# Kernel tuning notes

Hardware: AMD Instinct MI355X
Metric: run time of the kernel (lower is better)

The kernel has to match this reference:

```python
import jax, jax.numpy as jnp
import numpy as np

MARGIN = 0.3  # init kwarg, mode='norm'


def _pairwise_dist(X):
    # squared euclidean distances, then safe sqrt (matches euc_dist(X.t()).sqrt())
    sq = jnp.sum(X * X, axis=1)                      # [n]
    d2 = sq[:, None] + sq[None, :] - 2.0 * (X @ X.T)  # [n, n]
    d2 = jnp.maximum(d2, 0.0)
    # safe sqrt: avoid inf derivative at 0 (diagonal); forward value identical
    return jnp.where(d2 > 0.0, jnp.sqrt(jnp.where(d2 > 0.0, d2, 1.0)), 0.0)


def setup_inputs() -> dict:
    key = jax.random.key(0)
    kx, ky = jax.random.split(key)
    X = jax.random.normal(kx, (4096, 2048), dtype=jnp.float32)
    Y = jax.random.randint(ky, (4096,), 0, 128, dtype=jnp.int64)
    return {"X": X, "Y": Y}


def reference(X, Y):
    dist = _pairwise_dist(X)                         # [n, n]
    mask = Y[:, None] == Y[None, :]                  # same-identity mask [n, n]
    inf = jnp.array(jnp.inf, dtype=dist.dtype)
    # hardest positive per anchor: max over same-label entries
    dist_ap = jnp.max(jnp.where(mask, dist, -inf), axis=1)  # [n]
    # hardest negative per anchor: min over different-label entries
    dist_an = jnp.min(jnp.where(mask, inf, dist), axis=1)   # [n]
    # mode == 'norm': mean hinge
    return jnp.mean(jnp.maximum(dist_ap - dist_an + MARGIN, 0.0))
```

## Files before the change

### kernel.cpp

```cpp
#include <hip/hip_runtime.h>
#include <hip/hip_bf16.h>
#include <hip/hip_fp8.h>

typedef __attribute__((ext_vector_type(4))) int i32x4;
typedef __attribute__((ext_vector_type(8))) int i32x8;
typedef __attribute__((ext_vector_type(16))) float f32x16;

#define MARGIN 0.3f
#define BIGF 3.0e38f

__device__ __forceinline__ void gl2lds16(const void* g, void* l) {
    __builtin_amdgcn_global_load_lds(
        (const __attribute__((address_space(1))) void*)g,
        (__attribute__((address_space(3))) void*)l,
        16, 0, 0);
}

__global__ __launch_bounds__(256) void convert_norm_kernel(
    const float* __restrict__ X, unsigned char* __restrict__ Xq,
    float* __restrict__ nrm, unsigned* __restrict__ ap,
    unsigned* __restrict__ an, unsigned* __restrict__ cnt, int K) {
    const int wave = threadIdx.x >> 6, lane = threadIdx.x & 63;
    const int row = blockIdx.x * 4 + wave;
    const float* xr = X + (size_t)row * K;
    unsigned char* xqr = Xq + (size_t)row * K;
    float s = 0.0f;
    for (int c = lane * 8; c < K; c += 64 * 8) {
        float4 v0 = *(const float4*)(xr + c);
        float4 v1 = *(const float4*)(xr + c + 4);
        float f[8] = {v0.x, v0.y, v0.z, v0.w, v1.x, v1.y, v1.z, v1.w};
        union { unsigned char b[8]; uint2 u; } p;
#pragma unroll
        for (int i = 0; i < 8; i++) {
            __hip_fp8_e4m3 q(f[i]);
            p.b[i] = q.__x;
            float d = (float)q;
            s += d * d;
        }
        *(uint2*)(xqr + c) = p.u;
    }
    for (int off = 32; off > 0; off >>= 1) s += __shfl_xor(s, off, 64);
    if (lane == 0) {
        nrm[row] = s;
        ap[row] = 0u;
        an[row] = 0x7F800000u;
        if (row == 0) *cnt = 0u;
    }
}

__global__ __launch_bounds__(256, 4) void gemm_reduce_kernel(
    const unsigned char* __restrict__ Xq, const float* __restrict__ nrm,
    const int* __restrict__ Y, unsigned* __restrict__ ap,
    unsigned* __restrict__ an, unsigned* __restrict__ cnt,
    float* __restrict__ out, int N, int K) {
    __shared__ __align__(16) unsigned char sA[128 * 128];
    __shared__ __align__(16) unsigned char sB[128 * 128];
    __shared__ int sYr[128], sYc[128];
    __shared__ float sNr[128], sNc[128];
    __shared__ float redmax[4][64], redmin[4][64];
    __shared__ float lsum[4];
    __shared__ unsigned s_done;

    const int tid = threadIdx.x;
    const int wave = tid >> 6;
    const int lane = tid & 63;
    const int m = lane & 31;
    const int h = lane >> 5;
    const int wr = wave >> 1;
    const int wc = wave & 1;

    const int NB = N >> 7;
    const int rowBase = (blockIdx.x >> 5) * 128;
    const int colBase = (blockIdx.x & (NB - 1)) * 128;

    if (tid < 128) {
        sYr[tid] = Y[rowBase + tid];
        sNr[tid] = nrm[rowBase + tid];
    } else {
        int t = tid - 128;
        sYc[t] = Y[colBase + t];
        sNc[t] = nrm[colBase + t];
    }

    f32x16 acc[2][2];
#pragma unroll
    for (int si = 0; si < 2; si++)
#pragma unroll
        for (int sj = 0; sj < 2; sj++)
#pragma unroll
            for (int rr = 0; rr < 16; rr++) acc[si][sj][rr] = 0.0f;

    const int rsub = lane >> 3;
    const int jc = (lane & 7) ^ rsub;
    const unsigned char* gA = Xq + (size_t)(rowBase + wave * 32 + rsub) * K;
    const unsigned char* gB = Xq + (size_t)(colBase + wave * 32 + rsub) * K;
    unsigned char* lA = sA + wave * 4096;
    unsigned char* lB = sB + wave * 4096;
    const size_t g8 = (size_t)8 * K;

    const int e2 = (m & 7) ^ ((m >> 3) & 3);
    const int nit = K >> 7;

    for (int it = 0; it < nit; it++) {
        const size_t go = (size_t)it * 128;
#pragma unroll
        for (int g = 0; g < 4; g++) {
            gl2lds16(gA + go + g * g8 + ((jc ^ g) << 4), lA + g * 1024);
            gl2lds16(gB + go + g * g8 + ((jc ^ g) << 4), lB + g * 1024);
        }
        __syncthreads();

#pragma unroll
        for (int s = 0; s < 2; s++) {
            const int c0 = s * 4 + h * 2;
            i32x8 af[2], bf[2];
#pragma unroll
            for (int si = 0; si < 2; si++) {
                const unsigned char* base = sA + (wr * 64 + si * 32 + m) * 128;
                i32x4 lo = *(const i32x4*)(base + (((c0) ^ e2) << 4));
                i32x4 hi = *(const i32x4*)(base + (((c0 + 1) ^ e2) << 4));
                af[si] = __builtin_shufflevector(lo, hi, 0, 1, 2, 3, 4, 5, 6, 7);
            }
#pragma unroll
            for (int sj = 0; sj < 2; sj++) {
                const unsigned char* base = sB + (wc * 64 + sj * 32 + m) * 128;
                i32x4 lo = *(const i32x4*)(base + (((c0) ^ e2) << 4));
                i32x4 hi = *(const i32x4*)(base + (((c0 + 1) ^ e2) << 4));
                bf[sj] = __builtin_shufflevector(lo, hi, 0, 1, 2, 3, 4, 5, 6, 7);
            }
#pragma unroll
            for (int si = 0; si < 2; si++)
#pragma unroll
                for (int sj = 0; sj < 2; sj++)
                    acc[si][sj] = __builtin_amdgcn_mfma_scale_f32_32x32x64_f8f6f4(
                        af[si], bf[sj], acc[si][sj], 0 ,
                        0 , 0, 127 ,
                        0, 127 );
        }
        __syncthreads();
    }

#pragma unroll
    for (int si = 0; si < 2; si++)
#pragma unroll
        for (int reg = 0; reg < 16; reg++) {
            const int row64 = si * 32 + (reg & 3) + 8 * (reg >> 2) + 4 * h;
            const int rIdx = wr * 64 + row64;
            const int yr = sYr[rIdx];
            const float nr = sNr[rIdx];
            float dp = -1.0f, dn = BIGF;
#pragma unroll
            for (int sj = 0; sj < 2; sj++) {
                const int cIdx = wc * 64 + sj * 32 + m;
                float d2 = nr + sNc[cIdx] - 2.0f * acc[si][sj][reg];
                float d = sqrtf(fmaxf(d2, 0.0f));
                bool same = (yr == sYc[cIdx]);
                dp = fmaxf(dp, same ? d : -1.0f);
                dn = fminf(dn, same ? BIGF : d);
            }
            for (int off = 1; off < 32; off <<= 1) {
                dp = fmaxf(dp, __shfl_xor(dp, off, 64));
                dn = fminf(dn, __shfl_xor(dn, off, 64));
            }
            if (m == 0) {
                redmax[wave][row64] = dp;
                redmin[wave][row64] = dn;
            }
        }
    __syncthreads();

    if (tid < 128) {
        const int wr2 = tid >> 6, r64 = tid & 63;
        float mx = fmaxf(redmax[wr2 * 2][r64], redmax[wr2 * 2 + 1][r64]);
        float mn = fminf(redmin[wr2 * 2][r64], redmin[wr2 * 2 + 1][r64]);
        atomicMax(&ap[rowBase + tid], __float_as_uint(fmaxf(mx, 0.0f)));
        atomicMin(&an[rowBase + tid], __float_as_uint(mn));
    }

    __syncthreads();
    if (tid == 0) {
        __threadfence();
        s_done = atomicAdd(cnt, 1u);
    }
    __syncthreads();
    if (s_done == gridDim.x - 1) {
        __threadfence();
        float s = 0.0f;
        for (int i = tid; i < N; i += 256) {
            unsigned ua = __hip_atomic_load(&ap[i], __ATOMIC_RELAXED,
                                            __HIP_MEMORY_SCOPE_AGENT);
            unsigned ub = __hip_atomic_load(&an[i], __ATOMIC_RELAXED,
                                            __HIP_MEMORY_SCOPE_AGENT);
            s += fmaxf(__uint_as_float(ua) - __uint_as_float(ub) + MARGIN, 0.0f);
        }
        for (int off = 32; off > 0; off >>= 1) s += __shfl_xor(s, off, 64);
        if (lane == 0) lsum[wave] = s;
        __syncthreads();
        if (tid == 0)
            out[0] = (lsum[0] + lsum[1] + lsum[2] + lsum[3]) / (float)N;
    }
}

extern "C" void kernel_launch(void* const* d_in, const int* in_sizes, int n_in,
                              void* d_out, int out_size, void* d_ws, size_t ws_size,
                              hipStream_t stream) {
    const float* X = (const float*)d_in[0];
    const int* Y = (const int*)d_in[1];
    float* out = (float*)d_out;
    const int N = in_sizes[1];
    const int K = in_sizes[0] / N;

    char* ws = (char*)d_ws;
    unsigned char* Xq = (unsigned char*)ws;
    float* nrm = (float*)(ws + (size_t)N * K);
    unsigned* ap = (unsigned*)((char*)nrm + (size_t)N * 4);
    unsigned* an = (unsigned*)((char*)ap + (size_t)N * 4);
    unsigned* cnt = (unsigned*)((char*)an + (size_t)N * 4);

    convert_norm_kernel<<<N / 4, 256, 0, stream>>>(X, Xq, nrm, ap, an, cnt, K);
    const int NB = N / 128;
    gemm_reduce_kernel<<<NB * NB, 256, 0, stream>>>(Xq, nrm, Y, ap, an, cnt,
                                                    out, N, K);
}
```

Before: 132.9 us.

## Pre-swizzle FP8 operands into MFMA fragment layout and load directly from global

The conversion kernel now writes the FP8 matrix in a fragment-packed layout: 32-row panels, with each 64-wide K slice stored contiguously per lane. The GEMM drops LDS staging and per-iteration barriers, and each lane loads its 32-byte MFMA operands straight from global memory. This removes LDS traffic and synchronisation but gives up in-block reuse, so every wave fetches its own A and B fragments and relies on L2/L1 for reuse. An explicit barrier was added after the label and norm shared-memory loads.

```diff
diff --git a/kernel.cpp b/kernel.cpp
--- a/kernel.cpp
+++ b/kernel.cpp
@@ -9,21 +9,27 @@
 #define MARGIN 0.3f
 #define BIGF 3.0e38f
 
-__device__ __forceinline__ void gl2lds16(const void* g, void* l) {
-    __builtin_amdgcn_global_load_lds(
-        (const __attribute__((address_space(1))) void*)g,
-        (__attribute__((address_space(3))) void*)l,
-        16, 0, 0);
+__device__ __forceinline__ f32x16 mx_mfma(i32x8 a, i32x8 b, f32x16 c) {
+    return __builtin_amdgcn_mfma_scale_f32_32x32x64_f8f6f4(
+        a, b, c, 0 , 0 ,
+        0, 127 , 0, 127 );
+}
+
+__device__ __forceinline__ i32x8 ld32(const unsigned char* p) {
+    i32x4 lo = *(const i32x4*)p;
+    i32x4 hi = *(const i32x4*)(p + 16);
+    return __builtin_shufflevector(lo, hi, 0, 1, 2, 3, 4, 5, 6, 7);
 }
 
 __global__ __launch_bounds__(256) void convert_norm_kernel(
-    const float* __restrict__ X, unsigned char* __restrict__ Xq,
+    const float* __restrict__ X, unsigned char* __restrict__ Xf,
     float* __restrict__ nrm, unsigned* __restrict__ ap,
     unsigned* __restrict__ an, unsigned* __restrict__ cnt, int K) {
     const int wave = threadIdx.x >> 6, lane = threadIdx.x & 63;
     const int row = blockIdx.x * 4 + wave;
     const float* xr = X + (size_t)row * K;
-    unsigned char* xqr = Xq + (size_t)row * K;
+    const size_t pbase = ((size_t)(row >> 5)) << 16;
+    const int rsub = row & 31;
     float s = 0.0f;
     for (int c = lane * 8; c < K; c += 64 * 8) {
         float4 v0 = *(const float4*)(xr + c);
@@ -37,7 +43,10 @@
             float d = (float)q;
             s += d * d;
         }
-        *(uint2*)(xqr + c) = p.u;
+        const int lslot = rsub + (((c >> 5) & 1) << 5);
+        unsigned char* dst = Xf + pbase + ((size_t)(c >> 6) << 11)
+                             + (lslot << 5) + (c & 31);
+        *(uint2*)dst = p.u;
     }
     for (int off = 32; off > 0; off >>= 1) s += __shfl_xor(s, off, 64);
     if (lane == 0) {
@@ -49,12 +58,10 @@
 }
 
 __global__ __launch_bounds__(256, 4) void gemm_reduce_kernel(
-    const unsigned char* __restrict__ Xq, const float* __restrict__ nrm,
+    const unsigned char* __restrict__ Xf, const float* __restrict__ nrm,
     const int* __restrict__ Y, unsigned* __restrict__ ap,
     unsigned* __restrict__ an, unsigned* __restrict__ cnt,
     float* __restrict__ out, int N, int K) {
-    __shared__ __align__(16) unsigned char sA[128 * 128];
-    __shared__ __align__(16) unsigned char sB[128 * 128];
     __shared__ int sYr[128], sYc[128];
     __shared__ float sNr[128], sNc[128];
     __shared__ float redmax[4][64], redmin[4][64];
@@ -81,6 +88,7 @@
         sYc[t] = Y[colBase + t];
         sNc[t] = nrm[colBase + t];
     }
+    __syncthreads();
 
     f32x16 acc[2][2];
 #pragma unroll
@@ -90,54 +98,25 @@
 #pragma unroll
             for (int rr = 0; rr < 16; rr++) acc[si][sj][rr] = 0.0f;
 
-    const int rsub = lane >> 3;
-    const int jc = (lane & 7) ^ rsub;
-    const unsigned char* gA = Xq + (size_t)(rowBase + wave * 32 + rsub) * K;
-    const unsigned char* gB = Xq + (size_t)(colBase + wave * 32 + rsub) * K;
-    unsigned char* lA = sA + wave * 4096;
-    unsigned char* lB = sB + wave * 4096;
-    const size_t g8 = (size_t)8 * K;
-
-    const int e2 = (m & 7) ^ ((m >> 3) & 3);
-    const int nit = K >> 7;
-
-    for (int it = 0; it < nit; it++) {
-        const size_t go = (size_t)it * 128;
-#pragma unroll
-        for (int g = 0; g < 4; g++) {
-            gl2lds16(gA + go + g * g8 + ((jc ^ g) << 4), lA + g * 1024);
-            gl2lds16(gB + go + g * g8 + ((jc ^ g) << 4), lB + g * 1024);
-        }
-        __syncthreads();
-
-#pragma unroll
-        for (int s = 0; s < 2; s++) {
-            const int c0 = s * 4 + h * 2;
-            i32x8 af[2], bf[2];
-#pragma unroll
-            for (int si = 0; si < 2; si++) {
-                const unsigned char* base = sA + (wr * 64 + si * 32 + m) * 128;
-                i32x4 lo = *(const i32x4*)(base + (((c0) ^ e2) << 4));
-                i32x4 hi = *(const i32x4*)(base + (((c0 + 1) ^ e2) << 4));
-                af[si] = __builtin_shufflevector(lo, hi, 0, 1, 2, 3, 4, 5, 6, 7);
-            }
-#pragma unroll
-            for (int sj = 0; sj < 2; sj++) {
-                const unsigned char* base = sB + (wc * 64 + sj * 32 + m) * 128;
-                i32x4 lo = *(const i32x4*)(base + (((c0) ^ e2) << 4));
-                i32x4 hi = *(const i32x4*)(base + (((c0 + 1) ^ e2) << 4));
-                bf[sj] = __builtin_shufflevector(lo, hi, 0, 1, 2, 3, 4, 5, 6, 7);
-            }
-#pragma unroll
-            for (int si = 0; si < 2; si++)
-#pragma unroll
-                for (int sj = 0; sj < 2; sj++)
-                    acc[si][sj] = __builtin_amdgcn_mfma_scale_f32_32x32x64_f8f6f4(
-                        af[si], bf[sj], acc[si][sj], 0 ,
-                        0 , 0, 127 ,
-                        0, 127 );
-        }
-        __syncthreads();
+    const unsigned char* a0 =
+        Xf + (((size_t)(rowBase >> 5) + wr * 2) << 16) + lane * 32;
+    const unsigned char* a1 = a0 + 65536;
+    const unsigned char* b0 =
+        Xf + (((size_t)(colBase >> 5) + wc * 2) << 16) + lane * 32;
+    const unsigned char* b1 = b0 + 65536;
+
+    const int nt = K >> 6;
+#pragma unroll 4
+    for (int t = 0; t < nt; t++) {
+        const size_t off = (size_t)t << 11;
+        i32x8 af0 = ld32(a0 + off);
+        i32x8 af1 = ld32(a1 + off);
+        i32x8 bf0 = ld32(b0 + off);
+        i32x8 bf1 = ld32(b1 + off);
+        acc[0][0] = mx_mfma(af0, bf0, acc[0][0]);
+        acc[0][1] = mx_mfma(af0, bf1, acc[0][1]);
+        acc[1][0] = mx_mfma(af1, bf0, acc[1][0]);
+        acc[1][1] = mx_mfma(af1, bf1, acc[1][1]);
     }
 
 #pragma unroll
@@ -211,14 +190,14 @@
     const int K = in_sizes[0] / N;
 
     char* ws = (char*)d_ws;
-    unsigned char* Xq = (unsigned char*)ws;
+    unsigned char* Xf = (unsigned char*)ws;
     float* nrm = (float*)(ws + (size_t)N * K);
     unsigned* ap = (unsigned*)((char*)nrm + (size_t)N * 4);
     unsigned* an = (unsigned*)((char*)ap + (size_t)N * 4);
     unsigned* cnt = (unsigned*)((char*)an + (size_t)N * 4);
 
-    convert_norm_kernel<<<N / 4, 256, 0, stream>>>(X, Xq, nrm, ap, an, cnt, K);
+    convert_norm_kernel<<<N / 4, 256, 0, stream>>>(X, Xf, nrm, ap, an, cnt, K);
     const int NB = N / 128;
-    gemm_reduce_kernel<<<NB * NB, 256, 0, stream>>>(Xq, nrm, Y, ap, an, cnt,
+    gemm_reduce_kernel<<<NB * NB, 256, 0, stream>>>(Xf, nrm, Y, ap, an, cnt,
                                                     out, N, K);
 }
```

After: 132.9 us. Within noise of the previous version (+0.0%).
